# Performance work log

Measured on AMD Instinct MI355X. Metric: run time of the kernel, lower is better.

## Reference

```python
import jax, jax.numpy as jnp
import numpy as np

B, S, D, H = 2, 2048, 1024, 16
DK = D // H


def layernorm(x, gamma, bias, eps=1e-6):
    m = jnp.mean(x, axis=-1, keepdims=True)
    v = jnp.mean((x - m) ** 2, axis=-1, keepdims=True)  # biased var (correction=0)
    return gamma * (x - m) / jnp.sqrt(v + eps) + bias


def setup_inputs() -> dict:
    key = jax.random.key(0)
    ks = jax.random.split(key, 10)
    xav = (2.0 / (D + D)) ** 0.5  # xavier_normal_ std for square [D,D]
    lin1_b = (1.0 / D) ** 0.5     # nn.Linear default init bound
    lin2_b = (1.0 / (4 * D)) ** 0.5
    return {
        "X": jax.random.normal(ks[0], (B, S, D), jnp.float32),
        "padding_mask": jnp.ones((B, 1, S), jnp.int32),
        "W_Q": jax.random.normal(ks[1], (D, D), jnp.float32) * xav,
        "W_K": jax.random.normal(ks[2], (D, D), jnp.float32) * xav,
        "W_V": jax.random.normal(ks[3], (D, D), jnp.float32) * xav,
        "W_O": jax.random.normal(ks[4], (D, D), jnp.float32) * xav,
        "g1": jnp.ones((D,), jnp.float32),
        "b1": jnp.zeros((D,), jnp.float32),
        "W1": jax.random.uniform(ks[5], (D, 4 * D), jnp.float32, -lin1_b, lin1_b),
        "bias1": jax.random.uniform(ks[6], (4 * D,), jnp.float32, -lin1_b, lin1_b),
        "W2": jax.random.uniform(ks[7], (4 * D, D), jnp.float32, -lin2_b, lin2_b),
        "bias2": jax.random.uniform(ks[8], (D,), jnp.float32, -lin2_b, lin2_b),
        "g2": jnp.ones((D,), jnp.float32),
        "b2": jnp.zeros((D,), jnp.float32),
    }


def reference(X, padding_mask, W_Q, W_K, W_V, W_O, g1, b1, W1, bias1, W2, bias2, g2, b2):
    b, s, d = X.shape
    # pre-norm + MHA
    xn = layernorm(X, g1, b1)
    q = (xn @ W_Q).reshape(b, s, H, DK).transpose(0, 2, 1, 3)  # [B,H,S,DK]
    k = (xn @ W_K).reshape(b, s, H, DK).transpose(0, 2, 1, 3)
    v = (xn @ W_V).reshape(b, s, H, DK).transpose(0, 2, 1, 3)
    scores = jnp.einsum("bhqd,bhkd->bhqk", q, k) / np.sqrt(DK).astype(np.float32)
    mask = padding_mask[:, None, :, :]  # [B,1,1,S] broadcast over heads/queries
    scores = jnp.where(mask == 0, jnp.float32(-1e9), scores)
    w = jax.nn.softmax(scores, axis=-1)
    attn = jnp.einsum("bhqk,bhkd->bhqd", w, v)
    attn = attn.transpose(0, 2, 1, 3).reshape(b, s, d) @ W_O
    out = attn + X
    # pre-norm + GELU FFN (exact erf GELU, matching nn.GELU default)
    nn2 = layernorm(out, g2, b2)
    ff = jax.nn.gelu(nn2 @ W1 + bias1, approximate=False) @ W2 + bias2
    return ff + out
```

## Files before the change

kernel.cpp:

```cpp
#include <hip/hip_runtime.h>
#include <hip/hip_bf16.h>


using bf16 = __hip_bfloat16;
typedef __attribute__((ext_vector_type(4))) float f32x4;
typedef __attribute__((ext_vector_type(16))) float f32x16;
typedef __attribute__((ext_vector_type(8))) short bf16x8;

#define DEVI static __device__ __forceinline__

DEVI void async_copy16(const void* g, void* l) {
  __builtin_amdgcn_global_load_lds(
      (const __attribute__((address_space(1))) void*)g,
      (__attribute__((address_space(3))) void*)l, 16, 0, 0);
}

DEVI ushort f2bf_bits(float v) {
  __hip_bfloat16 h = __float2bfloat16(v);
  return *reinterpret_cast<ushort*>(&h);
}

DEVI float bfbits2f(ushort u) {
  union { float f; unsigned int i; } x;
  x.i = ((unsigned int)u) << 16;
  return x.f;
}

DEVI unsigned int pk2(float lo, float hi) {
  return (unsigned int)f2bf_bits(lo) | ((unsigned int)f2bf_bits(hi) << 16);
}

__global__ __launch_bounds__(256) void ln_kernel(
    const float* __restrict__ in, const float* __restrict__ gamma,
    const float* __restrict__ beta, bf16* __restrict__ out) {
  const long row = blockIdx.x;
  const int t = threadIdx.x;
  float4 x = ((const float4*)(in + row * 1024))[t];
  float s = x.x + x.y + x.z + x.w;
  float s2 = x.x * x.x + x.y * x.y + x.z * x.z + x.w * x.w;
#pragma unroll
  for (int m = 1; m < 64; m <<= 1) {
    s += __shfl_xor(s, m);
    s2 += __shfl_xor(s2, m);
  }
  __shared__ float red[8];
  const int w = t >> 6, l = t & 63;
  if (l == 0) { red[w] = s; red[4 + w] = s2; }
  __syncthreads();
  s = red[0] + red[1] + red[2] + red[3];
  s2 = red[4] + red[5] + red[6] + red[7];
  const float mean = s * (1.0f / 1024.0f);
  const float var = s2 * (1.0f / 1024.0f) - mean * mean;
  const float rstd = rsqrtf(var + 1e-6f);
  float4 g4 = ((const float4*)gamma)[t];
  float4 b4 = ((const float4*)beta)[t];
  union { ushort h[4]; uint2 u; } o;
  o.h[0] = f2bf_bits(g4.x * (x.x - mean) * rstd + b4.x);
  o.h[1] = f2bf_bits(g4.y * (x.y - mean) * rstd + b4.y);
  o.h[2] = f2bf_bits(g4.z * (x.z - mean) * rstd + b4.z);
  o.h[3] = f2bf_bits(g4.w * (x.w - mean) * rstd + b4.w);
  ((uint2*)(out + row * 1024))[t] = o.u;
}

__global__ __launch_bounds__(256) void transpose_all(
    const float* __restrict__ q, const float* __restrict__ k,
    const float* __restrict__ v, const float* __restrict__ o,
    const float* __restrict__ w1, const float* __restrict__ w2,
    bf16* __restrict__ wqkvo, bf16* __restrict__ w1t, bf16* __restrict__ w2t) {
  const int tid = blockIdx.x;
  const float* W;
  bf16* Wt;
  int K, N, n0, k0;
  if (tid < 4096) {
    const int z = tid >> 10, r = tid & 1023;
    W = (z == 0) ? q : (z == 1) ? k : (z == 2) ? v : o;
    Wt = wqkvo + (size_t)z * 1024 * 1024;
    K = 1024; N = 1024; n0 = (r & 31) << 5; k0 = (r >> 5) << 5;
  } else if (tid < 8192) {
    const int r = tid - 4096;
    W = w1; Wt = w1t; K = 1024; N = 4096;
    n0 = (r & 127) << 5; k0 = (r >> 7) << 5;
  } else {
    const int r = tid - 8192;
    W = w2; Wt = w2t; K = 4096; N = 1024;
    n0 = (r & 31) << 5; k0 = (r >> 5) << 5;
  }
  __shared__ float tile[32][33];
  const int tx = threadIdx.x & 31, ty = threadIdx.x >> 5;
#pragma unroll
  for (int i = 0; i < 32; i += 8)
    tile[ty + i][tx] = W[(long)(k0 + ty + i) * N + n0 + tx];
  __syncthreads();
#pragma unroll
  for (int i = 0; i < 32; i += 8)
    Wt[(long)(n0 + ty + i) * K + k0 + tx] = __float2bfloat16(tile[tx][ty + i]);
}

template <int EPI, int KSPLIT>
__global__ __launch_bounds__(256) void gemm_bt(
    const bf16* __restrict__ A, const bf16* __restrict__ Bt,
    const int M, const int N, const int K, const int lda, const int ldb,
    const float* __restrict__ bias, const float* __restrict__ res,
    float* __restrict__ pother, void* __restrict__ Cout) {
  __shared__ bf16 As[128 * 32];
  __shared__ bf16 Bs[128 * 32];
  const int t = threadIdx.x;
  const int w = t >> 6, l = t & 63;
  const int nb = N >> 7;
  const int cpx = gridDim.x >> 3;
  int bidx = (blockIdx.x & 7) * cpx + (blockIdx.x >> 3);
  int sl = 0;
  if (KSPLIT == 2) {
    const int half = gridDim.x >> 1;
    sl = bidx >= half;
    bidx -= sl * half;
  }
  const int bm = bidx / nb, bn = bidx % nb;
  const long row0 = (long)bm << 7, col0 = (long)bn << 7;
  const int wr = (w >> 1) << 6, wc = (w & 1) << 6;
  const int lr = l & 15, lk = (l >> 4) << 3;

  f32x4 acc[4][4];
#pragma unroll
  for (int m = 0; m < 4; ++m)
#pragma unroll
    for (int n = 0; n < 4; ++n) acc[m][n] = (f32x4){0.f, 0.f, 0.f, 0.f};

  const bf16* gA = A + (row0 + (t >> 2)) * (long)lda + (long)sl * K + ((t & 3) << 3);
  const bf16* gB = Bt + (col0 + (t >> 2)) * (long)ldb + (long)sl * K + ((t & 3) << 3);
  char* lA = (char*)As + (w << 10);
  char* lB = (char*)Bs + (w << 10);
  const long k64a = (long)64 * lda, k64b = (long)64 * ldb;

  for (int k0 = 0; k0 < K; k0 += 32) {
    __syncthreads();
    async_copy16(gA + k0, lA);
    async_copy16(gA + k64a + k0, lA + 4096);
    async_copy16(gB + k0, lB);
    async_copy16(gB + k64b + k0, lB + 4096);
    __syncthreads();
    bf16x8 af[4], bfr[4];
#pragma unroll
    for (int m = 0; m < 4; ++m)
      af[m] = *(const bf16x8*)&As[(wr + m * 16 + lr) * 32 + lk];
#pragma unroll
    for (int n = 0; n < 4; ++n)
      bfr[n] = *(const bf16x8*)&Bs[(wc + n * 16 + lr) * 32 + lk];
#pragma unroll
    for (int m = 0; m < 4; ++m)
#pragma unroll
      for (int n = 0; n < 4; ++n)
        acc[m][n] = __builtin_amdgcn_mfma_f32_16x16x32_bf16(af[m], bfr[n], acc[m][n], 0, 0, 0);
  }

  bf16* Cb = (bf16*)Cout;
  float* Cf = (float*)Cout;
  if (EPI == 5 && sl == 1) Cf = pother;
#pragma unroll
  for (int m = 0; m < 4; ++m) {
#pragma unroll
    for (int r = 0; r < 4; ++r) {
      const long crow = row0 + wr + m * 16 + ((l >> 4) << 2) + r;
      const long rbase = crow * N;
#pragma unroll
      for (int n = 0; n < 4; ++n) {
        const long ccol = col0 + wc + n * 16 + lr;
        float v = acc[m][n][r];
        if (EPI == 2) {
          const float vv = v + bias[ccol];
          const float u2 = vv * (1.5957691216f + 0.0713548162f * vv * vv);
          v = vv / (1.0f + __expf(-u2));
        }
        if (EPI == 1) v += res[rbase + ccol];
        if (EPI == 5 && sl == 0) v += bias[ccol] + res[rbase + ccol];
        if (EPI == 0 || EPI == 2)
          Cb[rbase + ccol] = __float2bfloat16(v);
        else
          Cf[rbase + ccol] = v;
      }
    }
  }
}

__global__ __launch_bounds__(256) void ff2_reduce(
    const float* __restrict__ p0, const float* __restrict__ p1,
    float* __restrict__ out) {
  const int idx = blockIdx.x * 256 + threadIdx.x;
  const float4 x = ((const float4*)p0)[idx];
  const float4 y = ((const float4*)p1)[idx];
  float4 a;
  a.x = x.x + y.x; a.y = x.y + y.y; a.z = x.z + y.z; a.w = x.w + y.w;
  ((float4*)out)[idx] = a;
}

__global__ __launch_bounds__(512) void attn_kernel(
    const bf16* __restrict__ QKV, const int* __restrict__ pmask,
    bf16* __restrict__ Oout) {
  const int bh = blockIdx.x;
  const int b = bh >> 4, h = bh & 15;
  const int q0 = blockIdx.y << 8;
  const int t = threadIdx.x;
  const int w = t >> 6, l = t & 63;
  const int lq = l & 31, hi = l >> 5;

  __shared__ __align__(16) char smem[65536];

  const long base = (long)b * 2048 * 3072;
  const bf16* Qg = QKV + base + h * 64;
  const bf16* Kg = QKV + base + 1024 + h * 64;
  const bf16* Vg = QKV + base + 2048 + h * 64;

  int kSrc[2], kDst[2], vk[2], vsg[2];
#pragma unroll
  for (int p = 0; p < 2; ++p) {
    const int c = p * 512 + t;
    const int kr = c >> 3;
    kSrc[p] = kr * 3072 + (((c & 7) ^ (kr & 7)) << 3);
    kDst[p] = c * 16;
    vk[p] = c >> 3;
    vsg[p] = c & 7;
  }

  const int qw0 = q0 + w * 32;
  bf16x8 qf[4];
#pragma unroll
  for (int dc = 0; dc < 4; ++dc) {
    uint4 raw = *(const uint4*)(Qg + (long)(qw0 + lq) * 3072 + dc * 16 + hi * 8);
    union { uint4 u4; ushort us[8]; } in; in.u4 = raw;
    union { bf16x8 v; ushort us[8]; } o;
#pragma unroll
    for (int e = 0; e < 8; ++e) o.us[e] = f2bf_bits(0.125f * bfbits2f(in.us[e]));
    qf[dc] = o.v;
  }

  union { unsigned int u[4]; bf16x8 v; } bones;
  bones.u[0] = (hi == 0) ? 0x00003F80u : 0u;
  bones.u[1] = bones.u[2] = bones.u[3] = 0u;

  uint4 vreg[2];
#pragma unroll
  for (int p = 0; p < 2; ++p) {
    vreg[p] = *(const uint4*)(Vg + (long)vk[p] * 3072 + vsg[p] * 8);
    async_copy16(Kg + kSrc[p], smem + kDst[p]);
  }
#pragma unroll
  for (int p = 0; p < 2; ++p) {
    const ushort* vs = (const ushort*)&vreg[p];
#pragma unroll
    for (int e = 0; e < 8; ++e) {
      const int d = vsg[p] * 8 + e;
      *(ushort*)(smem + 32768 + d * 256 +
                 ((vk[p] * 2) ^ (((e ^ vsg[p]) & 7) << 4))) = vs[e];
    }
  }

  f32x16 oacc[2];
#pragma unroll
  for (int nt = 0; nt < 2; ++nt)
#pragma unroll
    for (int r = 0; r < 16; ++r) oacc[nt][r] = 0.f;
  float mrun = -3.0e38f, lsum = 0.f;
  int cur = 0;

  __syncthreads();

  for (int ktg = 0; ktg < 16; ++ktg) {
    if (ktg < 15) {
      const long nrow0 = (long)(ktg + 1) * 128 * 3072;
#pragma unroll
      for (int p = 0; p < 2; ++p) {
        vreg[p] = *(const uint4*)(Vg + nrow0 + (long)vk[p] * 3072 + vsg[p] * 8);
        async_copy16(Kg + nrow0 + kSrc[p], smem + (cur ^ 1) * 16384 + kDst[p]);
      }
    }
    const int k0 = ktg << 7;
    const char* Ks = smem + cur * 16384;
    const char* Vt = smem + 32768 + cur * 16384;

    f32x16 sacc[4];
#pragma unroll
    for (int kt = 0; kt < 4; ++kt) {
#pragma unroll
      for (int r = 0; r < 16; ++r) sacc[kt][r] = 0.f;
#pragma unroll
      for (int dc = 0; dc < 4; ++dc) {
        bf16x8 ka = *(const bf16x8*)(Ks +
            ((kt * 32 + lq) * 128 + ((dc * 32 + hi * 16) ^ ((lq & 7) << 4))));
        sacc[kt] = __builtin_amdgcn_mfma_f32_32x32x16_bf16(ka, qf[dc], sacc[kt], 0, 0, 0);
      }
      const int mv = pmask[b * 2048 + k0 + kt * 32 + lq];
      union { unsigned int u[4]; bf16x8 v; } aadd;
      aadd.u[0] = (hi == 0 && mv == 0) ? (unsigned int)f2bf_bits(-1.0e9f) : 0u;
      aadd.u[1] = aadd.u[2] = aadd.u[3] = 0u;
      sacc[kt] = __builtin_amdgcn_mfma_f32_32x32x16_bf16(aadd.v, bones.v, sacc[kt], 0, 0, 0);
    }

    float tmax = -3.0e38f;
#pragma unroll
    for (int kt = 0; kt < 4; ++kt)
#pragma unroll
      for (int r = 0; r < 16; ++r) tmax = fmaxf(tmax, sacc[kt][r]);
    tmax = fmaxf(tmax, __shfl_xor(tmax, 32));
    const bool need = (bool)__any(tmax > mrun);
    const float mnew = need ? fmaxf(mrun, tmax) : mrun;
    float psum = 0.f;
#pragma unroll
    for (int kt = 0; kt < 4; ++kt)
#pragma unroll
      for (int r = 0; r < 16; ++r) {
        const float p = __expf(sacc[kt][r] - mnew);
        sacc[kt][r] = p;
        psum += p;
      }
    psum += __shfl_xor(psum, 32);
    if (need) {
      const float alpha = __expf(mrun - mnew);
      mrun = mnew;
      lsum = lsum * alpha + psum;
#pragma unroll
      for (int r = 0; r < 16; ++r) {
        const float ar = __shfl(alpha, (r & 3) + 8 * (r >> 2) + 4 * hi);
        oacc[0][r] *= ar;
        oacc[1][r] *= ar;
      }
    } else {
      lsum += psum;
    }

    union { unsigned int u[4]; bf16x8 v; } paE[4], paO[4];
#pragma unroll
    for (int kt = 0; kt < 4; ++kt) {
      const unsigned int cs0 = pk2(sacc[kt][0], sacc[kt][1]);
      const unsigned int cs1 = pk2(sacc[kt][2], sacc[kt][3]);
      const unsigned int cs2 = pk2(sacc[kt][4], sacc[kt][5]);
      const unsigned int cs3 = pk2(sacc[kt][6], sacc[kt][7]);
      const unsigned int cs4 = pk2(sacc[kt][8], sacc[kt][9]);
      const unsigned int cs5 = pk2(sacc[kt][10], sacc[kt][11]);
      const unsigned int cs6 = pk2(sacc[kt][12], sacc[kt][13]);
      const unsigned int cs7 = pk2(sacc[kt][14], sacc[kt][15]);
      const unsigned int es0 = __shfl_xor(cs0, 32);
      const unsigned int es1 = __shfl_xor(cs1, 32);
      const unsigned int es2 = __shfl_xor(cs2, 32);
      const unsigned int es3 = __shfl_xor(cs3, 32);
      const unsigned int es4 = __shfl_xor(cs4, 32);
      const unsigned int es5 = __shfl_xor(cs5, 32);
      const unsigned int es6 = __shfl_xor(cs6, 32);
      const unsigned int es7 = __shfl_xor(cs7, 32);
      paE[kt].u[0] = hi ? es2 : cs0;
      paE[kt].u[1] = hi ? es3 : cs1;
      paE[kt].u[2] = hi ? cs2 : es0;
      paE[kt].u[3] = hi ? cs3 : es1;
      paO[kt].u[0] = hi ? es6 : cs4;
      paO[kt].u[1] = hi ? es7 : cs5;
      paO[kt].u[2] = hi ? cs6 : es4;
      paO[kt].u[3] = hi ? cs7 : es5;
    }

#pragma unroll
    for (int kt = 0; kt < 4; ++kt)
#pragma unroll
      for (int nt = 0; nt < 2; ++nt) {
        const int vrow = nt * 32 + lq;
        const int vsw = ((vrow & 7) ^ ((vrow >> 3) & 7)) << 4;
        bf16x8 vbE = *(const bf16x8*)(Vt + (vrow * 256 + ((kt * 64 + hi * 16) ^ vsw)));
        oacc[nt] = __builtin_amdgcn_mfma_f32_32x32x16_bf16(paE[kt].v, vbE, oacc[nt], 0, 0, 0);
        bf16x8 vbO = *(const bf16x8*)(Vt + (vrow * 256 + ((kt * 64 + 32 + hi * 16) ^ vsw)));
        oacc[nt] = __builtin_amdgcn_mfma_f32_32x32x16_bf16(paO[kt].v, vbO, oacc[nt], 0, 0, 0);
      }

    if (ktg < 15) {
      char* VtN = smem + 32768 + (cur ^ 1) * 16384;
#pragma unroll
      for (int p = 0; p < 2; ++p) {
        const ushort* vs = (const ushort*)&vreg[p];
#pragma unroll
        for (int e = 0; e < 8; ++e) {
          const int d = vsg[p] * 8 + e;
          *(ushort*)(VtN + d * 256 +
                     ((vk[p] * 2) ^ (((e ^ vsg[p]) & 7) << 4))) = vs[e];
        }
      }
    }

    __syncthreads();
    cur ^= 1;
  }

  const float inv = 1.0f / lsum;
#pragma unroll
  for (int r = 0; r < 16; ++r) {
    const int crow = (r & 3) + 8 * (r >> 2) + 4 * hi;
    const float ir = __shfl(inv, crow);
    const long orow = (long)b * 2048 + qw0 + crow;
#pragma unroll
    for (int nt = 0; nt < 2; ++nt)
      Oout[orow * 1024 + h * 64 + nt * 32 + lq] = __float2bfloat16(oacc[nt][r] * ir);
  }
}

extern "C" void kernel_launch(void* const* d_in, const int* in_sizes, int n_in,
                              void* d_out, int out_size, void* d_ws, size_t ws_size,
                              hipStream_t stream) {
  const float* X = (const float*)d_in[0];
  const int* pmask = (const int*)d_in[1];
  const float* W_Q = (const float*)d_in[2];
  const float* W_K = (const float*)d_in[3];
  const float* W_V = (const float*)d_in[4];
  const float* W_O = (const float*)d_in[5];
  const float* g1 = (const float*)d_in[6];
  const float* b1 = (const float*)d_in[7];
  const float* W1 = (const float*)d_in[8];
  const float* bias1 = (const float*)d_in[9];
  const float* W2 = (const float*)d_in[10];
  const float* bias2 = (const float*)d_in[11];
  const float* g2 = (const float*)d_in[12];
  const float* b2 = (const float*)d_in[13];
  (void)in_sizes; (void)n_in; (void)out_size; (void)ws_size;

  char* ws = (char*)d_ws;
  const size_t MB = 1ull << 20;
  bf16* W1_t   = (bf16*)(ws + 0);
  bf16* Wqkv_t = (bf16*)(ws + 8 * MB);
  bf16* Wo_t   = (bf16*)(ws + 14 * MB);
  bf16* W2_t   = (bf16*)(ws + 16 * MB);
  bf16* xn     = (bf16*)(ws + 24 * MB);
  bf16* QKV    = (bf16*)(ws + 32 * MB);
  bf16* attnb  = (bf16*)(ws + 56 * MB);
  bf16* ff1    = (bf16*)(ws + 32 * MB);
  float* p0    = (float*)(ws + 64 * MB);
  float* p1    = (float*)(ws + 0);
  float* res1  = (float*)d_out;

  transpose_all<<<12288, 256, 0, stream>>>(W_Q, W_K, W_V, W_O, W1, W2,
                                           Wqkv_t, W1_t, W2_t);
  ln_kernel<<<4096, 256, 0, stream>>>(X, g1, b1, xn);
  gemm_bt<0, 1><<<32 * 24, 256, 0, stream>>>(xn, Wqkv_t, 4096, 3072, 1024, 1024, 1024,
                                             nullptr, nullptr, nullptr, QKV);
  attn_kernel<<<dim3(32, 8), 512, 0, stream>>>(QKV, pmask, attnb);
  gemm_bt<1, 1><<<32 * 8, 256, 0, stream>>>(attnb, Wo_t, 4096, 1024, 1024, 1024, 1024,
                                            nullptr, X, nullptr, res1);
  ln_kernel<<<4096, 256, 0, stream>>>(res1, g2, b2, xn);
  gemm_bt<2, 1><<<32 * 32, 256, 0, stream>>>(xn, W1_t, 4096, 4096, 1024, 1024, 1024,
                                             bias1, nullptr, nullptr, ff1);
  gemm_bt<5, 2><<<2 * 32 * 8, 256, 0, stream>>>(ff1, W2_t, 4096, 1024, 2048, 4096, 4096,
                                                bias2, res1, p1, p0);
  ff2_reduce<<<4096, 256, 0, stream>>>(p0, p1, res1);
}
```

Measured before the change: 305.7 us.

## Use BK=64 swizzled LDS tiles, split-K O-proj, fuse reduce with LayerNorm

The GEMM K-tile grows from 32 to 64, with an XOR swizzle on LDS rows to avoid bank conflicts, which halves the number of barrier pairs per K. The output projection now uses split-K 2 to give more blocks, and a new kernel fuses the partial-sum reduction, residual add and the second LayerNorm. This removes the separate residual epilogue and one full pass over the activation. The cost is more LDS per block and extra fp32 partial-buffer traffic.

```diff
diff --git a/kernel.cpp b/kernel.cpp
--- a/kernel.cpp
+++ b/kernel.cpp
@@ -60,6 +60,47 @@
   o.h[2] = f2bf_bits(g4.z * (x.z - mean) * rstd + b4.z);
   o.h[3] = f2bf_bits(g4.w * (x.w - mean) * rstd + b4.w);
   ((uint2*)(out + row * 1024))[t] = o.u;
+}
+
+__global__ __launch_bounds__(256) void oproj_reduce_ln(
+    const float* __restrict__ p0, const float* __restrict__ p1,
+    const float* __restrict__ X, const float* __restrict__ gamma,
+    const float* __restrict__ beta, float* __restrict__ res_out,
+    bf16* __restrict__ xn_out) {
+  const long row = blockIdx.x;
+  const int t = threadIdx.x;
+  const long i = row * 256 + t;
+  const float4 a = ((const float4*)p0)[i];
+  const float4 b = ((const float4*)p1)[i];
+  const float4 c = ((const float4*)X)[i];
+  float4 x;
+  x.x = a.x + b.x + c.x; x.y = a.y + b.y + c.y;
+  x.z = a.z + b.z + c.z; x.w = a.w + b.w + c.w;
+  ((float4*)res_out)[i] = x;
+  float s = x.x + x.y + x.z + x.w;
+  float s2 = x.x * x.x + x.y * x.y + x.z * x.z + x.w * x.w;
+#pragma unroll
+  for (int m = 1; m < 64; m <<= 1) {
+    s += __shfl_xor(s, m);
+    s2 += __shfl_xor(s2, m);
+  }
+  __shared__ float red[8];
+  const int w = t >> 6, l = t & 63;
+  if (l == 0) { red[w] = s; red[4 + w] = s2; }
+  __syncthreads();
+  s = red[0] + red[1] + red[2] + red[3];
+  s2 = red[4] + red[5] + red[6] + red[7];
+  const float mean = s * (1.0f / 1024.0f);
+  const float var = s2 * (1.0f / 1024.0f) - mean * mean;
+  const float rstd = rsqrtf(var + 1e-6f);
+  float4 g4 = ((const float4*)gamma)[t];
+  float4 b4 = ((const float4*)beta)[t];
+  union { ushort h[4]; uint2 u; } o;
+  o.h[0] = f2bf_bits(g4.x * (x.x - mean) * rstd + b4.x);
+  o.h[1] = f2bf_bits(g4.y * (x.y - mean) * rstd + b4.y);
+  o.h[2] = f2bf_bits(g4.z * (x.z - mean) * rstd + b4.z);
+  o.h[3] = f2bf_bits(g4.w * (x.w - mean) * rstd + b4.w);
+  ((uint2*)(xn_out + row * 1024))[t] = o.u;
 }
 
 __global__ __launch_bounds__(256) void transpose_all(
@@ -102,8 +143,8 @@
     const int M, const int N, const int K, const int lda, const int ldb,
     const float* __restrict__ bias, const float* __restrict__ res,
     float* __restrict__ pother, void* __restrict__ Cout) {
-  __shared__ bf16 As[128 * 32];
-  __shared__ bf16 Bs[128 * 32];
+  __shared__ bf16 As[128 * 64];
+  __shared__ bf16 Bs[128 * 64];
   const int t = threadIdx.x;
   const int w = t >> 6, l = t & 63;
   const int nb = N >> 7;
@@ -118,7 +159,8 @@
   const int bm = bidx / nb, bn = bidx % nb;
   const long row0 = (long)bm << 7, col0 = (long)bn << 7;
   const int wr = (w >> 1) << 6, wc = (w & 1) << 6;
-  const int lr = l & 15, lk = (l >> 4) << 3;
+  const int lr = l & 15;
+  const int lkb = (l >> 4) << 4;
 
   f32x4 acc[4][4];
 #pragma unroll
@@ -126,36 +168,47 @@
 #pragma unroll
     for (int n = 0; n < 4; ++n) acc[m][n] = (f32x4){0.f, 0.f, 0.f, 0.f};
 
-  const bf16* gA = A + (row0 + (t >> 2)) * (long)lda + (long)sl * K + ((t & 3) << 3);
-  const bf16* gB = Bt + (col0 + (t >> 2)) * (long)ldb + (long)sl * K + ((t & 3) << 3);
-  char* lA = (char*)As + (w << 10);
-  char* lB = (char*)Bs + (w << 10);
-  const long k64a = (long)64 * lda, k64b = (long)64 * ldb;
-
-  for (int k0 = 0; k0 < K; k0 += 32) {
+  const int rA = t >> 3;
+  const int g = (t & 7) ^ ((t >> 3) & 7);
+  const bf16* gA = A + (row0 + rA) * (long)lda + (long)sl * K + g * 8;
+  const bf16* gB = Bt + (col0 + rA) * (long)ldb + (long)sl * K + g * 8;
+  char* lA = (char*)As + t * 16;
+  char* lB = (char*)Bs + t * 16;
+
+  for (int k0 = 0; k0 < K; k0 += 64) {
     __syncthreads();
-    async_copy16(gA + k0, lA);
-    async_copy16(gA + k64a + k0, lA + 4096);
-    async_copy16(gB + k0, lB);
-    async_copy16(gB + k64b + k0, lB + 4096);
+#pragma unroll
+    for (int cr = 0; cr < 4; ++cr) {
+      async_copy16(gA + (long)cr * 32 * lda + k0, lA + cr * 4096);
+      async_copy16(gB + (long)cr * 32 * ldb + k0, lB + cr * 4096);
+    }
     __syncthreads();
-    bf16x8 af[4], bfr[4];
-#pragma unroll
-    for (int m = 0; m < 4; ++m)
-      af[m] = *(const bf16x8*)&As[(wr + m * 16 + lr) * 32 + lk];
-#pragma unroll
-    for (int n = 0; n < 4; ++n)
-      bfr[n] = *(const bf16x8*)&Bs[(wc + n * 16 + lr) * 32 + lk];
-#pragma unroll
-    for (int m = 0; m < 4; ++m)
-#pragma unroll
-      for (int n = 0; n < 4; ++n)
-        acc[m][n] = __builtin_amdgcn_mfma_f32_16x16x32_bf16(af[m], bfr[n], acc[m][n], 0, 0, 0);
+#pragma unroll
+    for (int ks = 0; ks < 2; ++ks) {
+      bf16x8 af[4], bfr[4];
+#pragma unroll
+      for (int m = 0; m < 4; ++m) {
+        const int row = wr + m * 16 + lr;
+        af[m] = *(const bf16x8*)((const char*)As +
+            (row * 128 + ((ks * 64 + lkb) ^ ((row & 7) << 4))));
+      }
+#pragma unroll
+      for (int n = 0; n < 4; ++n) {
+        const int row = wc + n * 16 + lr;
+        bfr[n] = *(const bf16x8*)((const char*)Bs +
+            (row * 128 + ((ks * 64 + lkb) ^ ((row & 7) << 4))));
+      }
+#pragma unroll
+      for (int m = 0; m < 4; ++m)
+#pragma unroll
+        for (int n = 0; n < 4; ++n)
+          acc[m][n] = __builtin_amdgcn_mfma_f32_16x16x32_bf16(af[m], bfr[n], acc[m][n], 0, 0, 0);
+    }
   }
 
   bf16* Cb = (bf16*)Cout;
   float* Cf = (float*)Cout;
-  if (EPI == 5 && sl == 1) Cf = pother;
+  if ((EPI == 4 || EPI == 5) && sl == 1) Cf = pother;
 #pragma unroll
   for (int m = 0; m < 4; ++m) {
 #pragma unroll
@@ -171,7 +224,6 @@
           const float u2 = vv * (1.5957691216f + 0.0713548162f * vv * vv);
           v = vv / (1.0f + __expf(-u2));
         }
-        if (EPI == 1) v += res[rbase + ccol];
         if (EPI == 5 && sl == 0) v += bias[ccol] + res[rbase + ccol];
         if (EPI == 0 || EPI == 2)
           Cb[rbase + ccol] = __float2bfloat16(v);
@@ -427,6 +479,8 @@
   bf16* QKV    = (bf16*)(ws + 32 * MB);
   bf16* attnb  = (bf16*)(ws + 56 * MB);
   bf16* ff1    = (bf16*)(ws + 32 * MB);
+  float* p0o   = (float*)(ws + 64 * MB);
+  float* p1o   = (float*)(ws + 32 * MB);
   float* p0    = (float*)(ws + 64 * MB);
   float* p1    = (float*)(ws + 0);
   float* res1  = (float*)d_out;
@@ -437,9 +491,9 @@
   gemm_bt<0, 1><<<32 * 24, 256, 0, stream>>>(xn, Wqkv_t, 4096, 3072, 1024, 1024, 1024,
                                              nullptr, nullptr, nullptr, QKV);
   attn_kernel<<<dim3(32, 8), 512, 0, stream>>>(QKV, pmask, attnb);
-  gemm_bt<1, 1><<<32 * 8, 256, 0, stream>>>(attnb, Wo_t, 4096, 1024, 1024, 1024, 1024,
-                                            nullptr, X, nullptr, res1);
-  ln_kernel<<<4096, 256, 0, stream>>>(res1, g2, b2, xn);
+  gemm_bt<4, 2><<<2 * 32 * 8, 256, 0, stream>>>(attnb, Wo_t, 4096, 1024, 512, 1024, 1024,
+                                                nullptr, nullptr, p1o, p0o);
+  oproj_reduce_ln<<<4096, 256, 0, stream>>>(p0o, p1o, X, g2, b2, res1, xn);
   gemm_bt<2, 1><<<32 * 32, 256, 0, stream>>>(xn, W1_t, 4096, 4096, 1024, 1024, 1024,
                                              bias1, nullptr, nullptr, ff1);
   gemm_bt<5, 2><<<2 * 32 * 8, 256, 0, stream>>>(ff1, W2_t, 4096, 1024, 2048, 4096, 4096,
```

Measured after the change: 289.7 us. 5.2% less time.
